# Kernel optimization log

Hardware: AMD Instinct MI355X
Metric: run time of the kernel (lower is better)

The kernel has to match this reference:

```python
import jax, jax.numpy as jnp
import numpy as np

B, S, D, H, DFF = 4, 2048, 1024, 16, 4096
DK = D // H
EPS = 1e-6


def setup_inputs() -> dict:
    key = jax.random.key(0)
    ks = jax.random.split(key, 20)
    p = lambda k, shape: jax.random.normal(k, shape, dtype=jnp.float32) * 0.02
    inp = {
        "x": jax.random.normal(ks[0], (B, S, D), dtype=jnp.float32),
        "src_mask": jax.random.randint(ks[1], (B, 1, 1, S), 0, 2, dtype=jnp.int32),
        "Wq": p(ks[2], (D, D)), "bq": jnp.zeros((D,), jnp.float32),
        "Wk": p(ks[3], (D, D)), "bk": jnp.zeros((D,), jnp.float32),
        "Wv": p(ks[4], (D, D)), "bv": jnp.zeros((D,), jnp.float32),
        "Wo": p(ks[5], (D, D)), "bo": jnp.zeros((D,), jnp.float32),
        "W1": p(ks[6], (D, DFF)), "b1": jnp.zeros((DFF,), jnp.float32),
        "W2": p(ks[7], (DFF, D)), "b2": jnp.zeros((D,), jnp.float32),
        "ln1_a": jnp.ones((D,), jnp.float32), "ln1_b": jnp.zeros((D,), jnp.float32),
        "ln2_a": jnp.ones((D,), jnp.float32), "ln2_b": jnp.zeros((D,), jnp.float32),
    }
    return inp


def _layer_norm(x, a, b):
    # Faithful to source: unbiased std (torch default) and divide by (std + eps)
    mean = jnp.mean(x, axis=-1, keepdims=True)
    std = jnp.std(x, axis=-1, ddof=1, keepdims=True)
    return a * (x - mean) / (std + EPS) + b


def reference(x, src_mask, Wq, bq, Wk, bk, Wv, bv, Wo, bo, W1, b1, W2, b2,
              ln1_a, ln1_b, ln2_a, ln2_b):
    # Multi-head self-attention (dropout = identity, eval mode)
    q = (x @ Wq + bq).reshape(B, S, H, DK)
    k = (x @ Wk + bk).reshape(B, S, H, DK)
    v = (x @ Wv + bv).reshape(B, S, H, DK)
    scores = jnp.einsum("bqhd,bkhd->bhqk", q, k) / jnp.sqrt(jnp.float32(DK))
    scores = jnp.where(src_mask == 0, jnp.float32(-1e9), scores)
    attn = jax.nn.softmax(scores, axis=-1)
    ctx = jnp.einsum("bhqk,bkhd->bqhd", attn, v).reshape(B, S, D)
    attn_out = ctx @ Wo + bo

    x = _layer_norm(x + attn_out, ln1_a, ln1_b)

    # FeedForward: linear -> relu -> (dropout=identity) -> linear
    ff = jax.nn.relu(x @ W1 + b1) @ W2 + b2
    x = _layer_norm(x + ff, ln2_a, ln2_b)
    return x
```

## Files before the change

kernel.cpp:

```cpp
#include <hip/hip_runtime.h>

#define Bn 4
#define Sn 2048
#define Dn 1024
#define Hn 16
#define DKn 64
#define DFFn 4096
#define Mn (Bn * Sn)
#define QKVS 3072

typedef __bf16 bf16;
typedef __attribute__((ext_vector_type(8))) __bf16 bf16x8;
typedef __attribute__((ext_vector_type(4))) __bf16 bf16x4;
typedef __attribute__((ext_vector_type(8))) unsigned short u16x8;
typedef __attribute__((ext_vector_type(4))) float f32x4;
typedef __attribute__((ext_vector_type(16))) float f32x16;

#define LOG2E_DIV8 0.18033688011112042f

__device__ __forceinline__ float exp2fast(float x) {
  return __builtin_amdgcn_exp2f(x);
}

__device__ __forceinline__ void glds16(const bf16* g, bf16* l) {
  __builtin_amdgcn_global_load_lds((const __attribute__((address_space(1))) void*)g,
                                   (__attribute__((address_space(3))) void*)l, 16, 0, 0);
}

__device__ __forceinline__ unsigned int pkbf16(float a, float b) {
  union { __bf16 h[2]; unsigned int u; } x;
  x.h[0] = (__bf16)a; x.h[1] = (__bf16)b;
  return x.u;
}

__global__ __launch_bounds__(256) void k_cvt_bf16(const float* __restrict__ in,
                                                  bf16* __restrict__ out) {
  size_t i = ((size_t)blockIdx.x * 256 + threadIdx.x) * 8;
  f32x4 a = *(const f32x4*)(in + i);
  f32x4 b = *(const f32x4*)(in + i + 4);
  bf16x8 o;
#pragma unroll
  for (int j = 0; j < 4; ++j) { o[j] = (bf16)a[j]; o[j + 4] = (bf16)b[j]; }
  *(bf16x8*)(out + i) = o;
}

__global__ __launch_bounds__(256) void k_prep(const float* __restrict__ Wq,
                                              const float* __restrict__ Wk,
                                              const float* __restrict__ Wv,
                                              const float* __restrict__ Wo,
                                              const float* __restrict__ W1,
                                              const float* __restrict__ W2,
                                              const float* __restrict__ bq,
                                              const float* __restrict__ bk,
                                              const float* __restrict__ bv,
                                              bf16* __restrict__ wqkvT,
                                              bf16* __restrict__ woT,
                                              bf16* __restrict__ w1T,
                                              bf16* __restrict__ w2T,
                                              float* __restrict__ bqkv) {
  __shared__ float tile[32][33];
  const int id = blockIdx.x, t = threadIdx.x;
  if (id >= 12288) {
    int j = (id - 12288) * 256 + t;
    float v = (j < 1024) ? bq[j] * LOG2E_DIV8
            : (j < 2048) ? bk[j - 1024] : bv[j - 2048];
    bqkv[j] = v;
    return;
  }
  const float* in;
  bf16* out;
  int K, N, bx, by;
  float scale = 1.f;
  if (id < 4096) {
    int z = id >> 10, local = id & 1023;
    bx = local & 31; by = local >> 5;
    K = Dn; N = Dn;
    if (z == 0)      { in = Wq; out = wqkvT; scale = LOG2E_DIV8; }
    else if (z == 1) { in = Wk; out = wqkvT + (size_t)1024 * Dn; }
    else if (z == 2) { in = Wv; out = wqkvT + (size_t)2048 * Dn; }
    else             { in = Wo; out = woT; }
  } else if (id < 8192) {
    int local = id - 4096;
    bx = local & 127; by = local >> 7;
    K = Dn; N = DFFn; in = W1; out = w1T;
  } else {
    int local = id - 8192;
    bx = local & 31; by = local >> 5;
    K = DFFn; N = Dn; in = W2; out = w2T;
  }
  const int n0 = bx * 32, k0 = by * 32;
  const int tx = t & 31, ty = t >> 5;
#pragma unroll
  for (int j = ty; j < 32; j += 8)
    tile[j][tx] = in[(size_t)(k0 + j) * N + n0 + tx];
  __syncthreads();
#pragma unroll
  for (int j = ty; j < 32; j += 8)
    out[(size_t)(n0 + j) * K + k0 + tx] = (bf16)(tile[tx][j] * scale);
}

__global__ __launch_bounds__(256) void k_vt(const bf16* __restrict__ v,
                                            bf16* __restrict__ vT, int vs) {
  __shared__ bf16 T[64][72];
  const int t = threadIdx.x;
  const int s0 = blockIdx.x * 64;
  const int bh = blockIdx.y, b = bh >> 4, h = bh & 15;
#pragma unroll
  for (int it = 0; it < 2; ++it) {
    int r = (t >> 3) + it * 32;
    int c = t & 7;
    u16x8 val = *(const u16x8*)(v + (size_t)(b * Sn + s0 + r) * vs + h * 64 + c * 8);
    *(u16x8*)&T[r][c * 8] = val;
  }
  __syncthreads();
#pragma unroll
  for (int it = 0; it < 2; ++it) {
    int d = (t >> 3) + it * 32;
    int cs = t & 7;
    bf16x8 o;
#pragma unroll
    for (int j = 0; j < 8; ++j) o[j] = T[cs * 8 + j][d];
    *(bf16x8*)(vT + ((size_t)bh * 64 + d) * Sn + s0 + cs * 8) = o;
  }
}

template <int NFRAG, int DO_RELU>
__global__ __launch_bounds__(512, 2) void k_gemm256(const bf16* __restrict__ A,
                                                    const bf16* __restrict__ BT,
                                                    const float* __restrict__ bias,
                                                    bf16* __restrict__ C,
                                                    int Ndim, int Kdim) {
  __shared__ __align__(128) bf16 Asm[2][256 * 64];
  __shared__ __align__(128) bf16 Bsm[2][NFRAG * 64 * 64];
  const int tid = threadIdx.x;
  const int wid = tid >> 6, lane = tid & 63;
  const int l15 = lane & 15, l4 = lane >> 4;
  const int wm = wid >> 2, wn = wid & 3;

  const int gx = gridDim.x;
  int lin = blockIdx.y * gx + blockIdx.x;
  const int nwg = gx * gridDim.y;
  lin = (lin & 7) * (nwg >> 3) + (lin >> 3);
  const int m0 = (lin / gx) * 256;
  const int n0 = (lin % gx) * (NFRAG * 64);

  f32x4 acc[8][NFRAG];
#pragma unroll
  for (int mf = 0; mf < 8; ++mf)
#pragma unroll
    for (int nf = 0; nf < NFRAG; ++nf) acc[mf][nf] = f32x4{0.f, 0.f, 0.f, 0.f};

  const int lr = lane >> 3, lc = lane & 7;
  const int NT = Kdim >> 6;

#define STAGE(buf, t)                                                              \
  {                                                                                \
    _Pragma("unroll") for (int it = 0; it < 4; ++it) {                             \
      int r = it * 64 + wid * 8 + lr;                                              \
      int ch = lc ^ (r & 7);                                                       \
      glds16(A + (size_t)(m0 + r) * Kdim + (size_t)(t) * 64 + ch * 8,              \
             &Asm[buf][(it * 64 + wid * 8) * 64]);                                 \
    }                                                                              \
    _Pragma("unroll") for (int it = 0; it < NFRAG; ++it) {                         \
      int r = it * 64 + wid * 8 + lr;                                              \
      int ch = lc ^ (r & 7);                                                       \
      glds16(BT + (size_t)(n0 + r) * Kdim + (size_t)(t) * 64 + ch * 8,             \
             &Bsm[buf][(it * 64 + wid * 8) * 64]);                                 \
    }                                                                              \
  }

  int p = 0;
  STAGE(0, 0);
  for (int t = 0; t < NT; ++t) {
    if (t + 1 < NT) {
      STAGE(p ^ 1, t + 1);
      if constexpr (NFRAG == 4) asm volatile("s_waitcnt vmcnt(8)" ::: "memory");
      else                      asm volatile("s_waitcnt vmcnt(6)" ::: "memory");
    } else {
      asm volatile("s_waitcnt vmcnt(0)" ::: "memory");
    }
    __builtin_amdgcn_sched_barrier(0);
    __builtin_amdgcn_s_barrier();

    bf16x8 bfrag[NFRAG][2];
#pragma unroll
    for (int nf = 0; nf < NFRAG; ++nf)
#pragma unroll
      for (int kk = 0; kk < 2; ++kk) {
        int r = wn * (NFRAG * 16) + nf * 16 + l15;
        int ch = (kk * 4 + l4) ^ (r & 7);
        bfrag[nf][kk] = *(const bf16x8*)&Bsm[p][r * 64 + ch * 8];
      }
#pragma unroll
    for (int half = 0; half < 2; ++half) {
      bf16x8 afr[4][2];
#pragma unroll
      for (int mf4 = 0; mf4 < 4; ++mf4)
#pragma unroll
        for (int kk = 0; kk < 2; ++kk) {
          int r = wm * 128 + half * 64 + mf4 * 16 + l15;
          int ch = (kk * 4 + l4) ^ (r & 7);
          afr[mf4][kk] = *(const bf16x8*)&Asm[p][r * 64 + ch * 8];
        }
      __builtin_amdgcn_s_setprio(1);
#pragma unroll
      for (int mf4 = 0; mf4 < 4; ++mf4)
#pragma unroll
        for (int nf = 0; nf < NFRAG; ++nf)
#pragma unroll
          for (int kk = 0; kk < 2; ++kk)
            acc[half * 4 + mf4][nf] = __builtin_amdgcn_mfma_f32_16x16x32_bf16(
                afr[mf4][kk], bfrag[nf][kk], acc[half * 4 + mf4][nf], 0, 0, 0);
      __builtin_amdgcn_s_setprio(0);
    }
    __builtin_amdgcn_s_barrier();
    p ^= 1;
  }
#undef STAGE

#pragma unroll
  for (int mf = 0; mf < 8; ++mf)
#pragma unroll
    for (int nf = 0; nf < NFRAG; ++nf) {
      int c = n0 + wn * (NFRAG * 16) + nf * 16 + l15;
      float bv = bias[c];
      int r0 = m0 + wm * 128 + mf * 16 + l4 * 4;
#pragma unroll
      for (int r = 0; r < 4; ++r) {
        float val = acc[mf][nf][r] + bv;
        if (DO_RELU) val = fmaxf(val, 0.f);
        C[(size_t)(r0 + r) * Ndim + c] = (bf16)val;
      }
    }
}

__global__ __launch_bounds__(512) void k_attn(const bf16* __restrict__ q,
                                              const bf16* __restrict__ k,
                                              const bf16* __restrict__ vT,
                                              const int* __restrict__ mask,
                                              bf16* __restrict__ ctx, int qs) {
  __shared__ __align__(128) bf16 Kt[2][64 * 64];
  __shared__ __align__(128) bf16 Vt[2][64 * 64];
  __shared__ float Mb[Sn];
  const int tid = threadIdx.x, wid = tid >> 6, lane = tid & 63;
  const int q31 = lane & 31, hi = lane >> 5;

  int lin = blockIdx.y * gridDim.x + blockIdx.x;
  lin = (lin & 7) * 64 + (lin >> 3);
  const int qblk = lin & 7, bh = lin >> 3;
  const int b = bh >> 4, h = bh & 15;
  const int q0 = qblk * 256 + wid * 32;

  for (int i = tid; i < Sn; i += 512)
    Mb[i] = mask[b * Sn + i] ? 0.f : -1.44269504e9f;

  bf16x8 qf[4];
#pragma unroll
  for (int t = 0; t < 4; ++t)
    qf[t] = *(const bf16x8*)(q + (size_t)(b * Sn + q0 + q31) * qs + h * 64 +
                             t * 16 + hi * 8);

  f32x16 o[2];
  o[0] = {}; o[1] = {};
  float mr = -INFINITY, lr = 0.f;

  const int lrow = lane >> 3;
  const int lch0 = lane & 7;
  const int sch = lch0 ^ (lrow ^ (wid & 3));

  for (int kb = 0; kb < Sn / 64; ++kb) {
    const int cur = kb & 1;
    if (kb == 0) {
      int row = wid * 8 + lrow;
      glds16(k + (size_t)(b * Sn + row) * qs + h * 64 + sch * 8, &Kt[0][wid * 512]);
      glds16(vT + ((size_t)bh * 64 + row) * Sn + sch * 8, &Vt[0][wid * 512]);
      __syncthreads();
    }
    if (kb + 1 < Sn / 64) {
      int row = wid * 8 + lrow;
      glds16(k + (size_t)(b * Sn + (kb + 1) * 64 + row) * qs + h * 64 + sch * 8,
             &Kt[cur ^ 1][wid * 512]);
      glds16(vT + ((size_t)bh * 64 + row) * Sn + (kb + 1) * 64 + sch * 8,
             &Vt[cur ^ 1][wid * 512]);
    }

    f32x16 sc[2];
#pragma unroll
    for (int kf = 0; kf < 2; ++kf)
#pragma unroll
      for (int rg = 0; rg < 4; ++rg) {
        f32x4 mb4 = *(const f32x4*)&Mb[kb * 64 + kf * 32 + rg * 8 + 4 * hi];
#pragma unroll
        for (int j = 0; j < 4; ++j) sc[kf][rg * 4 + j] = mb4[j];
      }
#pragma unroll
    for (int t = 0; t < 4; ++t) {
#pragma unroll
      for (int kf = 0; kf < 2; ++kf) {
        int row = kf * 32 + q31;
        int ch = (t * 2 + hi) ^ ((row & 7) ^ ((row >> 3) & 3));
        bf16x8 kfr = *(const bf16x8*)&Kt[cur][row * 64 + ch * 8];
        sc[kf] = __builtin_amdgcn_mfma_f32_32x32x16_bf16(kfr, qf[t], sc[kf], 0, 0, 0);
      }
    }

    float rmax = fmaxf(sc[0][0], sc[0][1]);
#pragma unroll
    for (int i = 2; i < 16; i += 2)
      rmax = fmaxf(fmaxf(rmax, sc[0][i]), sc[0][i + 1]);
#pragma unroll
    for (int i = 0; i < 16; i += 2)
      rmax = fmaxf(fmaxf(rmax, sc[1][i]), sc[1][i + 1]);
    rmax = fmaxf(rmax, __shfl_xor(rmax, 32));

    if (!__all(rmax <= mr + 8.f)) {
      float mnew = fmaxf(mr, rmax);
      float psc = exp2fast(mr - mnew);
      mr = mnew;
      lr *= psc;
#pragma unroll
      for (int af = 0; af < 2; ++af)
#pragma unroll
        for (int i = 0; i < 16; ++i) o[af][i] *= psc;
    }

    float psum = 0.f;
#pragma unroll
    for (int kf = 0; kf < 2; ++kf)
#pragma unroll
      for (int i = 0; i < 16; ++i) {
        float p = exp2fast(sc[kf][i] - mr);
        sc[kf][i] = p;
        psum += p;
      }
    psum += __shfl_xor(psum, 32);
    lr += psum;

#pragma unroll
    for (int ks = 0; ks < 4; ++ks) {
      const int kf = ks >> 1, R = (ks & 1) * 8;
      unsigned int a0 = pkbf16(sc[kf][R + 0], sc[kf][R + 1]);
      unsigned int a1 = pkbf16(sc[kf][R + 2], sc[kf][R + 3]);
      unsigned int b0 = pkbf16(sc[kf][R + 4], sc[kf][R + 5]);
      unsigned int b1 = pkbf16(sc[kf][R + 6], sc[kf][R + 7]);
      unsigned int sxa0 = __shfl_xor(a0, 32), sxa1 = __shfl_xor(a1, 32);
      unsigned int sxb0 = __shfl_xor(b0, 32), sxb1 = __shfl_xor(b1, 32);
      union { unsigned int w[4]; bf16x8 v; } pfu;
      pfu.w[0] = hi ? sxb0 : a0;
      pfu.w[1] = hi ? sxb1 : a1;
      pfu.w[2] = hi ? b0 : sxa0;
      pfu.w[3] = hi ? b1 : sxa1;
#pragma unroll
      for (int af = 0; af < 2; ++af) {
        int row = af * 32 + q31;
        int ch = (ks * 2 + hi) ^ ((row & 7) ^ ((row >> 3) & 3));
        bf16x8 vfr = *(const bf16x8*)&Vt[cur][row * 64 + ch * 8];
        o[af] = __builtin_amdgcn_mfma_f32_32x32x16_bf16(vfr, pfu.v, o[af], 0, 0, 0);
      }
    }
    __syncthreads();
  }

  float inv = 1.f / lr;
  const size_t cbase = (size_t)(b * Sn + q0 + q31) * Dn + h * 64;
#pragma unroll
  for (int af = 0; af < 2; ++af)
#pragma unroll
    for (int rg = 0; rg < 4; ++rg) {
      bf16x4 ov;
#pragma unroll
      for (int j = 0; j < 4; ++j) ov[j] = (bf16)(o[af][rg * 4 + j] * inv);
      *(bf16x4*)(ctx + cbase + af * 32 + rg * 8 + 4 * hi) = ov;
    }
}

template <int XF32, int OUTF32>
__global__ __launch_bounds__(256) void k_ln(const void* __restrict__ xp,
                                            const bf16* __restrict__ res,
                                            const float* __restrict__ gamma,
                                            const float* __restrict__ beta,
                                            void* __restrict__ yout) {
  const int row = blockIdx.x, t = threadIdx.x;
  const size_t base = (size_t)row * Dn + t * 4;
  f32x4 a;
  if constexpr (XF32) {
    a = *(const f32x4*)((const float*)xp + base);
  } else {
    bf16x4 x4 = *(const bf16x4*)((const bf16*)xp + base);
#pragma unroll
    for (int j = 0; j < 4; ++j) a[j] = (float)x4[j];
  }
  bf16x4 rb = *(const bf16x4*)(res + base);
  f32x4 vv;
#pragma unroll
  for (int j = 0; j < 4; ++j) vv[j] = a[j] + (float)rb[j];

  float s = vv[0] + vv[1] + vv[2] + vv[3];
#pragma unroll
  for (int off = 32; off; off >>= 1) s += __shfl_xor(s, off);
  __shared__ float red1[4], red2[4];
  if ((t & 63) == 0) red1[t >> 6] = s;
  __syncthreads();
  float mean = (red1[0] + red1[1] + red1[2] + red1[3]) * (1.f / 1024.f);

  float d[4], s2 = 0.f;
#pragma unroll
  for (int j = 0; j < 4; ++j) { d[j] = vv[j] - mean; s2 += d[j] * d[j]; }
#pragma unroll
  for (int off = 32; off; off >>= 1) s2 += __shfl_xor(s2, off);
  if ((t & 63) == 0) red2[t >> 6] = s2;
  __syncthreads();
  float var = (red2[0] + red2[1] + red2[2] + red2[3]) * (1.f / 1023.f);
  float inv = 1.f / (sqrtf(var) + 1e-6f);

  f32x4 g = *(const f32x4*)(gamma + t * 4);
  f32x4 bt = *(const f32x4*)(beta + t * 4);
#pragma unroll
  for (int j = 0; j < 4; ++j) d[j] = g[j] * d[j] * inv + bt[j];
  if constexpr (OUTF32) {
    f32x4 outv = {d[0], d[1], d[2], d[3]};
    *(f32x4*)((float*)yout + base) = outv;
  } else {
    bf16x4 outb;
#pragma unroll
    for (int j = 0; j < 4; ++j) outb[j] = (bf16)d[j];
    *(bf16x4*)((bf16*)yout + base) = outb;
  }
}

extern "C" void kernel_launch(void* const* d_in, const int* in_sizes, int n_in,
                              void* d_out, int out_size, void* d_ws, size_t ws_size,
                              hipStream_t stream) {
  const float* x   = (const float*)d_in[0];
  const int*   msk = (const int*)d_in[1];
  const float* Wq  = (const float*)d_in[2];
  const float* bq  = (const float*)d_in[3];
  const float* Wk  = (const float*)d_in[4];
  const float* bk  = (const float*)d_in[5];
  const float* Wv  = (const float*)d_in[6];
  const float* bv  = (const float*)d_in[7];
  const float* Wo  = (const float*)d_in[8];
  const float* bo  = (const float*)d_in[9];
  const float* W1  = (const float*)d_in[10];
  const float* b1  = (const float*)d_in[11];
  const float* W2  = (const float*)d_in[12];
  const float* b2  = (const float*)d_in[13];
  const float* g1  = (const float*)d_in[14];
  const float* be1 = (const float*)d_in[15];
  const float* g2  = (const float*)d_in[16];
  const float* be2 = (const float*)d_in[17];
  float* out = (float*)d_out;

  char* w = (char*)d_ws;
  size_t off = 0;
  auto alloc = [&](size_t bytes) { void* p = w + off; off += (bytes + 255) & ~(size_t)255; return p; };
  bf16* xb    = (bf16*)alloc((size_t)Mn * Dn * 2);
  bf16* wqkvT = (bf16*)alloc((size_t)QKVS * Dn * 2);
  bf16* woT   = (bf16*)alloc((size_t)Dn * Dn * 2);
  bf16* w1T   = (bf16*)alloc((size_t)Dn * DFFn * 2);
  bf16* w2T   = (bf16*)alloc((size_t)DFFn * Dn * 2);
  float* bqkv = (float*)alloc((size_t)QKVS * 4);
  bf16* qkv   = (bf16*)alloc((size_t)Mn * QKVS * 2);
  bf16* ctx   = (bf16*)alloc((size_t)Mn * Dn * 2);
  bf16* attnb = (bf16*)alloc((size_t)Mn * Dn * 2);
  bf16* yb    = (bf16*)alloc((size_t)Mn * Dn * 2);
  (void)ws_size; (void)in_sizes; (void)n_in; (void)out_size;
  bf16* vT = xb;
  bf16* hh = qkv;
  bf16* ff = xb;

  k_cvt_bf16<<<(Mn * Dn) / 2048, 256, 0, stream>>>(x, xb);
  k_prep<<<12300, 256, 0, stream>>>(Wq, Wk, Wv, Wo, W1, W2, bq, bk, bv,
                                    wqkvT, woT, w1T, w2T, bqkv);

  k_gemm256<4, 0><<<dim3(QKVS / 256, Mn / 256), 512, 0, stream>>>(xb, wqkvT, bqkv, qkv, QKVS, Dn);

  k_vt<<<dim3(Sn / 64, Bn * Hn), 256, 0, stream>>>(qkv + 2048, vT, QKVS);
  k_attn<<<dim3(Sn / 256, Bn * Hn), 512, 0, stream>>>(qkv, qkv + 1024, vT, msk, ctx, QKVS);

  k_gemm256<2, 0><<<dim3(Dn / 128, Mn / 256), 512, 0, stream>>>(ctx, woT, bo, attnb, Dn, Dn);

  k_ln<1, 0><<<Mn, 256, 0, stream>>>(x, attnb, g1, be1, yb);

  k_gemm256<4, 1><<<dim3(DFFn / 256, Mn / 256), 512, 0, stream>>>(yb, w1T, b1, hh, DFFn, Dn);

  k_gemm256<2, 0><<<dim3(Dn / 128, Mn / 256), 512, 0, stream>>>(hh, w2T, b2, ff, Dn, DFFn);

  k_ln<0, 1><<<Mn, 256, 0, stream>>>(yb, ff, g2, be2, out);
}
```

Before: 414.0 us.

## Add phased 256x256 GEMM kernel interleaving global loads with MFMA quadrants

Adds a new 256x256-tile GEMM kernel that splits each K-step into four MFMA quadrant phases. Each phase is separated by barriers and interleaves the next tile's async global-to-LDS loads in small chunks, with s_setprio raised around the MFMA blocks. Fragment registers are reused across phases to limit register pressure. The intent is to overlap memory traffic with tensor-core work in the QKV and FFN1 projections, at the cost of more barriers per K-step and a hand-tuned waitcnt schedule that must stay correct.

```diff
diff --git a/kernel.cpp b/kernel.cpp
--- a/kernel.cpp
+++ b/kernel.cpp
@@ -124,6 +124,161 @@
   }
 }
 
+template <int DO_RELU>
+__global__ __launch_bounds__(512, 2) void k_gemm8ph(const bf16* __restrict__ A,
+                                                    const bf16* __restrict__ BT,
+                                                    const float* __restrict__ bias,
+                                                    bf16* __restrict__ C,
+                                                    int Ndim, int Kdim) {
+  __shared__ __align__(128) bf16 Asm[2][256 * 64];
+  __shared__ __align__(128) bf16 Bsm[2][256 * 64];
+  const int tid = threadIdx.x;
+  const int wid = tid >> 6, lane = tid & 63;
+  const int l15 = lane & 15, l4 = lane >> 4;
+  const int wm = wid >> 2, wn = wid & 3;
+
+  const int gx = gridDim.x;
+  int lin = blockIdx.y * gx + blockIdx.x;
+  const int nwg = gx * gridDim.y;
+  lin = (lin & 7) * (nwg >> 3) + (lin >> 3);
+  const int m0 = (lin / gx) * 256;
+  const int n0 = (lin % gx) * 256;
+
+  f32x4 acc[8][4];
+#pragma unroll
+  for (int mf = 0; mf < 8; ++mf)
+#pragma unroll
+    for (int nf = 0; nf < 4; ++nf) acc[mf][nf] = f32x4{0.f, 0.f, 0.f, 0.f};
+
+  const int lr = lane >> 3, lc = lane & 7;
+  const int NT = Kdim >> 6;
+
+#define STGA(buf, t, it)                                                          \
+  { int r_ = (it) * 64 + wid * 8 + lr; int ch_ = lc ^ (r_ & 7);                   \
+    glds16(A + (size_t)(m0 + r_) * Kdim + (size_t)(t) * 64 + ch_ * 8,             \
+           &Asm[buf][((it) * 64 + wid * 8) * 64]); }
+#define STGB(buf, t, it)                                                          \
+  { int r_ = (it) * 64 + wid * 8 + lr; int ch_ = lc ^ (r_ & 7);                   \
+    glds16(BT + (size_t)(n0 + r_) * Kdim + (size_t)(t) * 64 + ch_ * 8,            \
+           &Bsm[buf][((it) * 64 + wid * 8) * 64]); }
+
+#pragma unroll
+  for (int it = 0; it < 4; ++it) { STGA(0, 0, it); STGB(0, 0, it); }
+
+  bf16x8 af[4][2], bl[2][2], bh2[2][2];
+
+  for (int j = 0; j < NT; ++j) {
+    const int d = j & 1, nb = d ^ 1;
+    const bool st = (j + 1 < NT);
+
+    if (st) {
+      STGA(nb, j + 1, 0); STGA(nb, j + 1, 1);
+      asm volatile("s_waitcnt vmcnt(2)" ::: "memory");
+    } else {
+      asm volatile("s_waitcnt vmcnt(0)" ::: "memory");
+    }
+    __builtin_amdgcn_s_barrier();
+#pragma unroll
+    for (int mf = 0; mf < 4; ++mf)
+#pragma unroll
+      for (int kk = 0; kk < 2; ++kk) {
+        int row = wm * 128 + mf * 16 + l15;
+        int ch = (kk * 4 + l4) ^ (row & 7);
+        af[mf][kk] = *(const bf16x8*)&Asm[d][row * 64 + ch * 8];
+      }
+#pragma unroll
+    for (int nf = 0; nf < 2; ++nf)
+#pragma unroll
+      for (int kk = 0; kk < 2; ++kk) {
+        int row = wn * 64 + nf * 16 + l15;
+        int ch = (kk * 4 + l4) ^ (row & 7);
+        bl[nf][kk] = *(const bf16x8*)&Bsm[d][row * 64 + ch * 8];
+      }
+    __builtin_amdgcn_s_setprio(1);
+#pragma unroll
+    for (int mf = 0; mf < 4; ++mf)
+#pragma unroll
+      for (int nf = 0; nf < 2; ++nf)
+#pragma unroll
+        for (int kk = 0; kk < 2; ++kk)
+          acc[mf][nf] = __builtin_amdgcn_mfma_f32_16x16x32_bf16(af[mf][kk], bl[nf][kk],
+                                                                acc[mf][nf], 0, 0, 0);
+    __builtin_amdgcn_s_setprio(0);
+
+    if (st) { STGA(nb, j + 1, 2); STGA(nb, j + 1, 3); }
+    __builtin_amdgcn_s_barrier();
+#pragma unroll
+    for (int nf = 0; nf < 2; ++nf)
+#pragma unroll
+      for (int kk = 0; kk < 2; ++kk) {
+        int row = wn * 64 + (2 + nf) * 16 + l15;
+        int ch = (kk * 4 + l4) ^ (row & 7);
+        bh2[nf][kk] = *(const bf16x8*)&Bsm[d][row * 64 + ch * 8];
+      }
+    __builtin_amdgcn_s_setprio(1);
+#pragma unroll
+    for (int mf = 0; mf < 4; ++mf)
+#pragma unroll
+      for (int nf = 0; nf < 2; ++nf)
+#pragma unroll
+        for (int kk = 0; kk < 2; ++kk)
+          acc[mf][2 + nf] = __builtin_amdgcn_mfma_f32_16x16x32_bf16(af[mf][kk], bh2[nf][kk],
+                                                                    acc[mf][2 + nf], 0, 0, 0);
+    __builtin_amdgcn_s_setprio(0);
+
+    if (st) { STGB(nb, j + 1, 0); STGB(nb, j + 1, 1); }
+    __builtin_amdgcn_s_barrier();
+#pragma unroll
+    for (int mf = 0; mf < 4; ++mf)
+#pragma unroll
+      for (int kk = 0; kk < 2; ++kk) {
+        int row = wm * 128 + 64 + mf * 16 + l15;
+        int ch = (kk * 4 + l4) ^ (row & 7);
+        af[mf][kk] = *(const bf16x8*)&Asm[d][row * 64 + ch * 8];
+      }
+    __builtin_amdgcn_s_setprio(1);
+#pragma unroll
+    for (int mf = 0; mf < 4; ++mf)
+#pragma unroll
+      for (int nf = 0; nf < 2; ++nf)
+#pragma unroll
+        for (int kk = 0; kk < 2; ++kk)
+          acc[4 + mf][2 + nf] = __builtin_amdgcn_mfma_f32_16x16x32_bf16(
+              af[mf][kk], bh2[nf][kk], acc[4 + mf][2 + nf], 0, 0, 0);
+    __builtin_amdgcn_s_setprio(0);
+
+    if (st) { STGB(nb, j + 1, 2); STGB(nb, j + 1, 3); }
+    __builtin_amdgcn_s_barrier();
+    __builtin_amdgcn_s_setprio(1);
+#pragma unroll
+    for (int mf = 0; mf < 4; ++mf)
+#pragma unroll
+      for (int nf = 0; nf < 2; ++nf)
+#pragma unroll
+        for (int kk = 0; kk < 2; ++kk)
+          acc[4 + mf][nf] = __builtin_amdgcn_mfma_f32_16x16x32_bf16(
+              af[mf][kk], bl[nf][kk], acc[4 + mf][nf], 0, 0, 0);
+    __builtin_amdgcn_s_setprio(0);
+  }
+#undef STGA
+#undef STGB
+
+#pragma unroll
+  for (int mf = 0; mf < 8; ++mf)
+#pragma unroll
+    for (int nf = 0; nf < 4; ++nf) {
+      int c = n0 + wn * 64 + nf * 16 + l15;
+      float bv = bias[c];
+      int r0 = m0 + wm * 128 + mf * 16 + l4 * 4;
+#pragma unroll
+      for (int r = 0; r < 4; ++r) {
+        float val = acc[mf][nf][r] + bv;
+        if (DO_RELU) val = fmaxf(val, 0.f);
+        C[(size_t)(r0 + r) * Ndim + c] = (bf16)val;
+      }
+    }
+}
+
 template <int NFRAG, int DO_RELU>
 __global__ __launch_bounds__(512, 2) void k_gemm256(const bf16* __restrict__ A,
                                                     const bf16* __restrict__ BT,
@@ -473,7 +628,7 @@
   k_prep<<<12300, 256, 0, stream>>>(Wq, Wk, Wv, Wo, W1, W2, bq, bk, bv,
                                     wqkvT, woT, w1T, w2T, bqkv);
 
-  k_gemm256<4, 0><<<dim3(QKVS / 256, Mn / 256), 512, 0, stream>>>(xb, wqkvT, bqkv, qkv, QKVS, Dn);
+  k_gemm8ph<0><<<dim3(QKVS / 256, Mn / 256), 512, 0, stream>>>(xb, wqkvT, bqkv, qkv, QKVS, Dn);
 
   k_vt<<<dim3(Sn / 64, Bn * Hn), 256, 0, stream>>>(qkv + 2048, vT, QKVS);
   k_attn<<<dim3(Sn / 256, Bn * Hn), 512, 0, stream>>>(qkv, qkv + 1024, vT, msk, ctx, QKVS);
@@ -482,7 +637,7 @@
 
   k_ln<1, 0><<<Mn, 256, 0, stream>>>(x, attnb, g1, be1, yb);
 
-  k_gemm256<4, 1><<<dim3(DFFn / 256, Mn / 256), 512, 0, stream>>>(yb, w1T, b1, hh, DFFn, Dn);
+  k_gemm8ph<1><<<dim3(DFFn / 256, Mn / 256), 512, 0, stream>>>(yb, w1T, b1, hh, DFFn, Dn);
 
   k_gemm256<2, 0><<<dim3(Dn / 128, Mn / 256), 512, 0, stream>>>(hh, w2T, b2, ff, Dn, DFFn);
 
```

Result: no change. 416.2 us (+0.5%).
